# Performance work log

Hardware: AMD Instinct MI355X
Metric: run time of the kernel (lower is better)

The kernel has to match this reference:

```python
import jax, jax.numpy as jnp
import numpy as np

HIDDEN = 1024
HEADS = 16
HEAD_DIM = HIDDEN // HEADS
EPS = 1e-5


def setup_inputs() -> dict:
    key = jax.random.key(0)
    ks = jax.random.split(key, 12)
    B, S, H = 2, 2048, HIDDEN
    s = 1.0 / np.sqrt(H)
    x = jax.random.normal(ks[0], (B, S, H), dtype=jnp.float32)
    Wq = jax.random.normal(ks[1], (H, H), dtype=jnp.float32) * s
    bq = jnp.zeros((H,), dtype=jnp.float32)
    Wk = jax.random.normal(ks[2], (H, H), dtype=jnp.float32) * s
    bk = jnp.zeros((H,), dtype=jnp.float32)
    Wv = jax.random.normal(ks[3], (H, H), dtype=jnp.float32) * s
    bv = jnp.zeros((H,), dtype=jnp.float32)
    Wg = jax.random.normal(ks[4], (2 * H, H), dtype=jnp.float32) * (1.0 / np.sqrt(2 * H))
    bg = jnp.zeros((H,), dtype=jnp.float32)
    gamma = jnp.ones((H,), dtype=jnp.float32)
    beta = jnp.zeros((H,), dtype=jnp.float32)
    return {"x": x, "Wq": Wq, "bq": bq, "Wk": Wk, "bk": bk, "Wv": Wv, "bv": bv,
            "Wg": Wg, "bg": bg, "gamma": gamma, "beta": beta}


def reference(x, Wq, bq, Wk, bk, Wv, bv, Wg, bg, gamma, beta):
    B, S, H = x.shape
    def heads(t):  # [B,S,H] -> [B,nH,S,hd]
        return t.reshape(B, S, HEADS, HEAD_DIM).transpose(0, 2, 1, 3)
    Q = heads(x @ Wq + bq)
    K = heads(x @ Wk + bk)
    V = heads(x @ Wv + bv)
    scores = jnp.einsum('bhqd,bhkd->bhqk', Q, K) / jnp.sqrt(jnp.float32(HEAD_DIM))
    flow = scores - scores.transpose(0, 1, 3, 2)  # antisymmetric
    w = jax.nn.softmax(flow, axis=-1)
    flowed = jnp.einsum('bhqk,bhkd->bhqd', w, V)
    flowed = flowed.transpose(0, 2, 1, 3).reshape(B, S, H)
    gate = jax.nn.sigmoid(jnp.concatenate([x, flowed], axis=-1) @ Wg + bg)
    y = x + gate * flowed
    mu = jnp.mean(y, axis=-1, keepdims=True)
    var = jnp.mean(jnp.square(y - mu), axis=-1, keepdims=True)
    return (y - mu) * jax.lax.rsqrt(var + EPS) * gamma + beta
```

## Files before the change

kernel.cpp:

```cpp
#include <hip/hip_runtime.h>
#include <hip/hip_bf16.h>

#define S_LEN 2048
#define NHEAD 16
#define HDIM 64
#define HID 1024

typedef __attribute__((ext_vector_type(8))) short bf16x8;
typedef __attribute__((ext_vector_type(4))) float f32x4;
typedef __attribute__((ext_vector_type(4))) unsigned int u32x4;
typedef __attribute__((ext_vector_type(2))) unsigned int u32x2;

__device__ __forceinline__ unsigned short f2bf(float x) {
    unsigned int u = __builtin_bit_cast(unsigned int, x);
    u = (u + 0x7fffu + ((u >> 16) & 1u)) >> 16;
    return (unsigned short)u;
}
__device__ __forceinline__ float bf2f(unsigned short s) {
    unsigned int u = ((unsigned int)s) << 16;
    return __builtin_bit_cast(float, u);
}
__device__ __forceinline__ unsigned cvtpk_bf16(float lo, float hi) {
    unsigned r;
    asm("v_cvt_pk_bf16_f32 %0, %1, %2" : "=v"(r) : "v"(lo), "v"(hi));
    return r;
}
__device__ __forceinline__ void gload16(const short* g, short* l) {
    __builtin_amdgcn_global_load_lds(
        (const __attribute__((address_space(1))) unsigned int*)g,
        (__attribute__((address_space(3))) unsigned int*)l, 16, 0, 0);
}
__device__ __forceinline__ bf16x8 negbf8(bf16x8 v) {
    u32x4 u = __builtin_bit_cast(u32x4, v);
    #pragma unroll
    for (int e = 0; e < 4; e++) u[e] ^= 0x80008000u;
    return __builtin_bit_cast(bf16x8, u);
}

#define QSCALE 0.1803368801111168f

__global__ void cvt_kernel(const float* __restrict__ src, short* __restrict__ dst, int n4) {
    int i = blockIdx.x * blockDim.x + threadIdx.x;
    if (i < n4) {
        float4 v = reinterpret_cast<const float4*>(src)[i];
        short4 o;
        o.x = (short)f2bf(v.x); o.y = (short)f2bf(v.y);
        o.z = (short)f2bf(v.z); o.w = (short)f2bf(v.w);
        reinterpret_cast<short4*>(dst)[i] = o;
    }
}

__global__ void transpose_all(const float* __restrict__ Wq, const float* __restrict__ Wk,
                              const float* __restrict__ Wv, const float* __restrict__ Wg,
                              short* __restrict__ WT, short* __restrict__ WgT) {
    __shared__ float tile[32][33];
    int z = blockIdx.z;
    const float* src; short* dst; int R;
    if (z == 0)      { src = Wq; dst = WT;               R = 1024; }
    else if (z == 1) { src = Wk; dst = WT + 1024 * 1024; R = 1024; }
    else if (z == 2) { src = Wv; dst = WT + 2 * 1024 * 1024; R = 1024; }
    else             { src = Wg; dst = WgT;              R = 2048; }
    int by = blockIdx.y * 32;
    if (by >= R) return;
    int bx = blockIdx.x * 32;
    const int C = 1024;
    int tx = threadIdx.x, ty = threadIdx.y;
    #pragma unroll
    for (int i = ty; i < 32; i += 8)
        tile[i][tx] = src[(size_t)(by + i) * C + bx + tx];
    __syncthreads();
    #pragma unroll
    for (int i = ty; i < 32; i += 8)
        dst[(size_t)(bx + i) * R + by + tx] = (short)f2bf(tile[tx][i]);
}

__global__ __launch_bounds__(256, 2)
void gemm_qkv(const short* __restrict__ xb, const short* __restrict__ WT,
              const float* __restrict__ bq, const float* __restrict__ bk,
              const float* __restrict__ bv,
              short* __restrict__ Qb, short* __restrict__ Kb, short* __restrict__ VT) {
    __shared__ short Al[2][128 * 32];
    __shared__ short Bl[2][128 * 32];
    int mb = blockIdx.x, nb = blockIdx.y;
    int tid = threadIdx.x;
    int wave = tid >> 6, lane = tid & 63;
    int wm = wave >> 1, wn = wave & 1;
    int lr = lane & 15, lg = lane >> 4;

    int r = tid >> 2;
    int c = tid & 3;
    int sc = (c ^ (r & 3)) * 8;
    int dst0 = tid * 8;
    int dst1 = (tid + 256) * 8;
    const short* a0 = xb + (size_t)(mb * 128 + r) * 1024 + sc;
    const short* a1 = a0 + (size_t)64 * 1024;
    const short* b0 = WT + (size_t)(nb * 128 + r) * 1024 + sc;
    const short* b1 = b0 + (size_t)64 * 1024;
    int fsw = (lg ^ (lr & 3)) * 8;

    f32x4 acc[4][4] = {};

    for (int ks = 0; ks < 16; ++ks) {
        int kg = ks * 64;
        __syncthreads();
        gload16(a0 + kg,      &Al[0][dst0]);
        gload16(a1 + kg,      &Al[0][dst1]);
        gload16(a0 + kg + 32, &Al[1][dst0]);
        gload16(a1 + kg + 32, &Al[1][dst1]);
        gload16(b0 + kg,      &Bl[0][dst0]);
        gload16(b1 + kg,      &Bl[0][dst1]);
        gload16(b0 + kg + 32, &Bl[1][dst0]);
        gload16(b1 + kg + 32, &Bl[1][dst1]);
        __syncthreads();
        #pragma unroll
        for (int s = 0; s < 2; s++) {
            bf16x8 af[4], bfr[4];
            #pragma unroll
            for (int t = 0; t < 4; t++)
                af[t] = *(bf16x8*)&Al[s][(wm * 64 + t * 16 + lr) * 32 + fsw];
            #pragma unroll
            for (int t = 0; t < 4; t++)
                bfr[t] = *(bf16x8*)&Bl[s][(wn * 64 + t * 16 + lr) * 32 + fsw];
            #pragma unroll
            for (int i = 0; i < 4; i++)
                #pragma unroll
                for (int jn = 0; jn < 4; jn++)
                    acc[i][jn] = __builtin_amdgcn_mfma_f32_16x16x32_bf16(af[i], bfr[jn], acc[i][jn], 0, 0, 0);
        }
    }

    int which = (nb * 128) >> 10;
    #pragma unroll
    for (int jn = 0; jn < 4; jn++) {
        int n = nb * 128 + wn * 64 + jn * 16 + lr;
        int n1 = n & 1023;
        if (which < 2) {
            const float* bias = (which == 0) ? bq : bk;
            short* out = (which == 0) ? Qb : Kb;
            float scale = (which == 0) ? QSCALE : 1.0f;
            float bv_ = bias[n1];
            #pragma unroll
            for (int i = 0; i < 4; i++) {
                #pragma unroll
                for (int j = 0; j < 4; j++) {
                    int mm = mb * 128 + wm * 64 + i * 16 + lg * 4 + j;
                    out[(size_t)mm * 1024 + n1] = (short)f2bf(acc[i][jn][j] * scale + bv_ * scale);
                }
            }
        } else {
            int h = n1 >> 6, dv = n1 & 63;
            float bv_ = bv[n1];
            #pragma unroll
            for (int i = 0; i < 4; i++) {
                int mm0 = mb * 128 + wm * 64 + i * 16 + lg * 4;
                int bb = mm0 >> 11, ss = mm0 & 2047;
                short4 vvv;
                vvv.x = (short)f2bf(acc[i][jn][0] + bv_);
                vvv.y = (short)f2bf(acc[i][jn][1] + bv_);
                vvv.z = (short)f2bf(acc[i][jn][2] + bv_);
                vvv.w = (short)f2bf(acc[i][jn][3] + bv_);
                *(short4*)&VT[((size_t)((bb * 16 + h) * 64 + dv)) * S_LEN + ss] = vvv;
            }
        }
    }
}

__global__ __launch_bounds__(256, 4)
void attn_kernel(const short* __restrict__ Qb, const short* __restrict__ Kb,
                 const short* __restrict__ VT, short* __restrict__ Fb) {
    __shared__ short Kt[64 * 64];
    __shared__ short Qt[64 * 64];
    __shared__ short Vt[64 * 64];
    __shared__ short Pl[4][16 * 64];

    int bid = (blockIdx.x & 7) * 128 + (blockIdx.x >> 3);
    int qb = bid & 31;
    int bh = bid >> 5;
    int b = bh >> 4, h = bh & 15;
    int tid = threadIdx.x;
    int wave = tid >> 6, lane = tid & 63;
    int lr = lane & 15, lg = lane >> 4;

    size_t rowbase = ((size_t)(b * S_LEN + qb * 64 + wave * 16 + lr)) * HID + h * HDIM;
    bf16x8 Qf[2], Kf[2];
    #pragma unroll
    for (int cc = 0; cc < 2; cc++) {
        Qf[cc] = *(const bf16x8*)(Qb + rowbase + cc * 32 + lg * 8);
        Kf[cc] = negbf8(*(const bf16x8*)(Kb + rowbase + cc * 32 + lg * 8));
    }

    int r0 = tid >> 3;
    int c = tid & 7;
    int swz = (c ^ (r0 & 7)) * 8;
    int dst0 = r0 * 64 + swz;
    int dst1 = (r0 + 32) * 64 + swz;
    const short* kp = Kb + (size_t)(b * S_LEN + r0) * HID + h * HDIM + c * 8;
    const short* qp = Qb + (size_t)(b * S_LEN + r0) * HID + h * HDIM + c * 8;
    const short* vp = VT + (size_t)bh * HDIM * S_LEN + (size_t)r0 * S_LEN + c * 8;

    bf16x8 kv0 = *(const bf16x8*)kp;
    bf16x8 kv1 = *(const bf16x8*)(kp + 32 * HID);
    bf16x8 qv0 = *(const bf16x8*)qp;
    bf16x8 qv1 = *(const bf16x8*)(qp + 32 * HID);
    bf16x8 vv0 = *(const bf16x8*)vp;
    bf16x8 vv1 = *(const bf16x8*)(vp + 32 * S_LEN);
    kp += 64 * HID; qp += 64 * HID; vp += 64;

    f32x4 O[4] = {};
    float m = -1e30f, l = 0.f;

    for (int kt = 0; kt < 32; ++kt) {
        __syncthreads();
        *(bf16x8*)&Kt[dst0] = kv0;
        *(bf16x8*)&Kt[dst1] = kv1;
        *(bf16x8*)&Qt[dst0] = qv0;
        *(bf16x8*)&Qt[dst1] = qv1;
        *(bf16x8*)&Vt[dst0] = vv0;
        *(bf16x8*)&Vt[dst1] = vv1;
        __syncthreads();

        if (kt < 31) {
            kv0 = *(const bf16x8*)kp;
            kv1 = *(const bf16x8*)(kp + 32 * HID);
            qv0 = *(const bf16x8*)qp;
            qv1 = *(const bf16x8*)(qp + 32 * HID);
            vv0 = *(const bf16x8*)vp;
            vv1 = *(const bf16x8*)(vp + 32 * S_LEN);
            kp += 64 * HID; qp += 64 * HID; vp += 64;
        }

        f32x4 S[4] = {};
        __builtin_amdgcn_s_setprio(1);
        #pragma unroll
        for (int t = 0; t < 4; t++) {
            #pragma unroll
            for (int c2 = 0; c2 < 2; c2++) {
                int fo = (t * 16 + lr) * 64 + (((4 * c2 + lg) ^ (lr & 7)) * 8);
                bf16x8 kf = *(bf16x8*)&Kt[fo];
                bf16x8 qf = *(bf16x8*)&Qt[fo];
                S[t] = __builtin_amdgcn_mfma_f32_16x16x32_bf16(kf, Qf[c2], S[t], 0, 0, 0);
                S[t] = __builtin_amdgcn_mfma_f32_16x16x32_bf16(qf, Kf[c2], S[t], 0, 0, 0);
            }
        }
        __builtin_amdgcn_s_setprio(0);

        float pm = -1e30f;
        #pragma unroll
        for (int t = 0; t < 4; t++)
            #pragma unroll
            for (int j = 0; j < 4; j++) pm = fmaxf(pm, S[t][j]);
        pm = fmaxf(pm, __shfl_xor(pm, 16));
        pm = fmaxf(pm, __shfl_xor(pm, 32));

        if (__any(pm > m + 8.f)) {
            float mn = fmaxf(m, pm);
            float alpha = exp2f(m - mn);
            m = mn;
            l *= alpha;
            float a[4];
            #pragma unroll
            for (int j = 0; j < 4; j++) a[j] = __shfl(alpha, lg * 4 + j);
            #pragma unroll
            for (int dvt = 0; dvt < 4; dvt++)
                #pragma unroll
                for (int j = 0; j < 4; j++) O[dvt][j] *= a[j];
        }

        unsigned Pd[4][2];
        float rs = 0.f;
        #pragma unroll
        for (int t = 0; t < 4; t++) {
            float p0 = exp2f(S[t][0] - m);
            float p1 = exp2f(S[t][1] - m);
            float p2 = exp2f(S[t][2] - m);
            float p3 = exp2f(S[t][3] - m);
            rs += (p0 + p1) + (p2 + p3);
            Pd[t][0] = cvtpk_bf16(p0, p1);
            Pd[t][1] = cvtpk_bf16(p2, p3);
        }
        rs += __shfl_xor(rs, 16);
        rs += __shfl_xor(rs, 32);
        l += rs;
        #pragma unroll
        for (int t = 0; t < 4; t++) {
            u32x2 pw;
            pw[0] = Pd[t][0];
            pw[1] = Pd[t][1];
            int po = lr * 64 + (((2 * t + (lg >> 1)) ^ (lr & 7)) * 8) + (lg & 1) * 4;
            *(u32x2*)&Pl[wave][po] = pw;
        }

        __builtin_amdgcn_s_setprio(1);
        #pragma unroll
        for (int c2 = 0; c2 < 2; c2++) {
            bf16x8 pf = *(bf16x8*)&Pl[wave][lr * 64 + (((4 * c2 + lg) ^ (lr & 7)) * 8)];
            #pragma unroll
            for (int dvt = 0; dvt < 4; dvt++) {
                bf16x8 vf = *(bf16x8*)&Vt[(dvt * 16 + lr) * 64 + (((4 * c2 + lg) ^ (lr & 7)) * 8)];
                O[dvt] = __builtin_amdgcn_mfma_f32_16x16x32_bf16(pf, vf, O[dvt], 0, 0, 0);
            }
        }
        __builtin_amdgcn_s_setprio(0);
    }

    float linv = 1.f / l;
    float li[4];
    #pragma unroll
    for (int j = 0; j < 4; j++) li[j] = __shfl(linv, lg * 4 + j);
    #pragma unroll
    for (int dvt = 0; dvt < 4; dvt++) {
        #pragma unroll
        for (int j = 0; j < 4; j++) {
            int q = qb * 64 + wave * 16 + lg * 4 + j;
            int dv = dvt * 16 + lr;
            Fb[((size_t)(b * S_LEN + q)) * HID + h * HDIM + dv] =
                (short)f2bf(O[dvt][j] * li[j]);
        }
    }
}

__global__ __launch_bounds__(256, 4)
void gemm_gate(const short* __restrict__ xb, const short* __restrict__ fb,
               const short* __restrict__ WgT, const float* __restrict__ bg,
               const float* __restrict__ x, float* __restrict__ y) {
    __shared__ short Al[2][64 * 32];
    __shared__ short Bl[2][64 * 32];
    int mb = blockIdx.x, nb = blockIdx.y;
    int tid = threadIdx.x;
    int wave = tid >> 6, lane = tid & 63;
    int wm = wave >> 1, wn = wave & 1;
    int lr = lane & 15, lg = lane >> 4;

    int r = tid >> 2;
    int c = tid & 3;
    int sc = (c ^ (r & 3)) * 8;
    int dst0 = tid * 8;
    size_t arow = (size_t)(mb * 64 + r) * 1024 + sc;
    const short* b0 = WgT + (size_t)(nb * 64 + r) * 2048 + sc;
    int fsw = (lg ^ (lr & 3)) * 8;

    f32x4 acc[2][2] = {};

    for (int ks = 0; ks < 32; ++ks) {
        int kg = ks * 64;
        const short* A = (kg < 1024) ? (xb + kg) : (fb + (kg - 1024));
        __syncthreads();
        gload16(A + arow, &Al[0][dst0]);
        gload16(A + arow + 32, &Al[1][dst0]);
        gload16(b0 + kg, &Bl[0][dst0]);
        gload16(b0 + kg + 32, &Bl[1][dst0]);
        __syncthreads();
        bf16x8 af[2][2], bfr[2][2];
        #pragma unroll
        for (int t = 0; t < 2; t++)
            #pragma unroll
            for (int s = 0; s < 2; s++) {
                af[t][s]  = *(bf16x8*)&Al[s][(wm * 32 + t * 16 + lr) * 32 + fsw];
                bfr[t][s] = *(bf16x8*)&Bl[s][(wn * 32 + t * 16 + lr) * 32 + fsw];
            }
        #pragma unroll
        for (int i = 0; i < 2; i++)
            #pragma unroll
            for (int jn = 0; jn < 2; jn++)
                #pragma unroll
                for (int s = 0; s < 2; s++)
                    acc[i][jn] = __builtin_amdgcn_mfma_f32_16x16x32_bf16(af[i][s], bfr[jn][s], acc[i][jn], 0, 0, 0);
    }

    #pragma unroll
    for (int jn = 0; jn < 2; jn++) {
        int n = nb * 64 + wn * 32 + jn * 16 + lr;
        float bgv = bg[n];
        #pragma unroll
        for (int i = 0; i < 2; i++) {
            #pragma unroll
            for (int j = 0; j < 4; j++) {
                int mm = mb * 64 + wm * 32 + i * 16 + lg * 4 + j;
                size_t idx = (size_t)mm * 1024 + n;
                float z = acc[i][jn][j] + bgv;
                float gate = 1.f / (1.f + __expf(-z));
                float fv = bf2f((unsigned short)fb[idx]);
                y[idx] = x[idx] + gate * fv;
            }
        }
    }
}

__global__ __launch_bounds__(256)
void ln_kernel(float* __restrict__ y, const float* __restrict__ gamma,
               const float* __restrict__ beta) {
    int row = blockIdx.x;
    int tid = threadIdx.x;
    float4 v4 = *(const float4*)&y[(size_t)row * 1024 + tid * 4];
    float v[4] = {v4.x, v4.y, v4.z, v4.w};
    float s = v[0] + v[1] + v[2] + v[3];
    float s2 = v[0]*v[0] + v[1]*v[1] + v[2]*v[2] + v[3]*v[3];
    #pragma unroll
    for (int off = 1; off < 64; off <<= 1) {
        s += __shfl_xor(s, off);
        s2 += __shfl_xor(s2, off);
    }
    __shared__ float red[8];
    int wave = tid >> 6, lane = tid & 63;
    if (lane == 0) { red[wave] = s; red[4 + wave] = s2; }
    __syncthreads();
    s = red[0] + red[1] + red[2] + red[3];
    s2 = red[4] + red[5] + red[6] + red[7];
    float mu = s * (1.f / 1024.f);
    float var = s2 * (1.f / 1024.f) - mu * mu;
    float rsq = rsqrtf(var + 1e-5f);
    float4 o4;
    float* o = (float*)&o4;
    #pragma unroll
    for (int e = 0; e < 4; e++) {
        int n = tid * 4 + e;
        o[e] = (v[e] - mu) * rsq * gamma[n] + beta[n];
    }
    *(float4*)&y[(size_t)row * 1024 + tid * 4] = o4;
}

extern "C" void kernel_launch(void* const* d_in, const int* in_sizes, int n_in,
                              void* d_out, int out_size, void* d_ws, size_t ws_size,
                              hipStream_t stream) {
    const float* x     = (const float*)d_in[0];
    const float* Wq    = (const float*)d_in[1];
    const float* bq    = (const float*)d_in[2];
    const float* Wk    = (const float*)d_in[3];
    const float* bk    = (const float*)d_in[4];
    const float* Wv    = (const float*)d_in[5];
    const float* bv    = (const float*)d_in[6];
    const float* Wg    = (const float*)d_in[7];
    const float* bg    = (const float*)d_in[8];
    const float* gamma = (const float*)d_in[9];
    const float* beta  = (const float*)d_in[10];
    float* out = (float*)d_out;

    char* w = (char*)d_ws;
    const size_t MB = 1024 * 1024;
    short* xb  = (short*)(w + 0 * MB);
    short* Qb  = (short*)(w + 8 * MB);
    short* Kb  = (short*)(w + 16 * MB);
    short* WT  = (short*)(w + 32 * MB);
    short* WgT = (short*)(w + 38 * MB);
    short* fb  = (short*)(w + 42 * MB);
    short* VT  = (short*)(w + 50 * MB);

    cvt_kernel<<<4096, 256, 0, stream>>>(x, xb, 4096 * 1024 / 4);
    dim3 tb(32, 8);
    transpose_all<<<dim3(32, 64, 4), tb, 0, stream>>>(Wq, Wk, Wv, Wg, WT, WgT);
    gemm_qkv<<<dim3(32, 24), 256, 0, stream>>>(xb, WT, bq, bk, bv, Qb, Kb, VT);
    attn_kernel<<<1024, 256, 0, stream>>>(Qb, Kb, VT, fb);
    gemm_gate<<<dim3(64, 16), 256, 0, stream>>>(xb, fb, WgT, bg, x, out);
    ln_kernel<<<4096, 256, 0, stream>>>(out, gamma, beta);
}
```

Before: 171.3 us.

## Double-buffer K/Q shared tiles and restructure attention loop synchronization

Splits the K and Q shared-memory tiles into two buffers. The next tile's K/Q is written into the alternate buffer while the current one feeds the score MFMAs, and the global prefetch is moved to after the score computation. Barriers now sit between the P store and the PV product, and at the end of each iteration, instead of around the tile stores. The goal is to let the QK^T MFMAs start without waiting on a barrier after the stores. In exchange it uses more LDS, and it issues unconditional prefetches past the last tile, which read beyond the sequence and possibly beyond the buffer end.

```diff
diff --git a/kernel.cpp b/kernel.cpp
--- a/kernel.cpp
+++ b/kernel.cpp
@@ -168,8 +168,8 @@
 __global__ __launch_bounds__(256, 4)
 void attn_kernel(const short* __restrict__ Qb, const short* __restrict__ Kb,
                  const short* __restrict__ VT, short* __restrict__ Fb) {
-    __shared__ short Kt[64 * 64];
-    __shared__ short Qt[64 * 64];
+    __shared__ short Kt[2][64 * 64];
+    __shared__ short Qt[2][64 * 64];
     __shared__ short Vt[64 * 64];
     __shared__ short Pl[4][16 * 64];
 
@@ -204,30 +204,30 @@
     bf16x8 qv1 = *(const bf16x8*)(qp + 32 * HID);
     bf16x8 vv0 = *(const bf16x8*)vp;
     bf16x8 vv1 = *(const bf16x8*)(vp + 32 * S_LEN);
+    *(bf16x8*)&Kt[0][dst0] = kv0;
+    *(bf16x8*)&Kt[0][dst1] = kv1;
+    *(bf16x8*)&Qt[0][dst0] = qv0;
+    *(bf16x8*)&Qt[0][dst1] = qv1;
     kp += 64 * HID; qp += 64 * HID; vp += 64;
+    kv0 = *(const bf16x8*)kp;
+    kv1 = *(const bf16x8*)(kp + 32 * HID);
+    qv0 = *(const bf16x8*)qp;
+    qv1 = *(const bf16x8*)(qp + 32 * HID);
+    kp += 64 * HID; qp += 64 * HID;
 
     f32x4 O[4] = {};
     float m = -1e30f, l = 0.f;
+    int pb = 0;
+
+    __syncthreads();
 
     for (int kt = 0; kt < 32; ++kt) {
-        __syncthreads();
-        *(bf16x8*)&Kt[dst0] = kv0;
-        *(bf16x8*)&Kt[dst1] = kv1;
-        *(bf16x8*)&Qt[dst0] = qv0;
-        *(bf16x8*)&Qt[dst1] = qv1;
         *(bf16x8*)&Vt[dst0] = vv0;
         *(bf16x8*)&Vt[dst1] = vv1;
-        __syncthreads();
-
-        if (kt < 31) {
-            kv0 = *(const bf16x8*)kp;
-            kv1 = *(const bf16x8*)(kp + 32 * HID);
-            qv0 = *(const bf16x8*)qp;
-            qv1 = *(const bf16x8*)(qp + 32 * HID);
-            vv0 = *(const bf16x8*)vp;
-            vv1 = *(const bf16x8*)(vp + 32 * S_LEN);
-            kp += 64 * HID; qp += 64 * HID; vp += 64;
-        }
+        *(bf16x8*)&Kt[pb ^ 1][dst0] = kv0;
+        *(bf16x8*)&Kt[pb ^ 1][dst1] = kv1;
+        *(bf16x8*)&Qt[pb ^ 1][dst0] = qv0;
+        *(bf16x8*)&Qt[pb ^ 1][dst1] = qv1;
 
         f32x4 S[4] = {};
         __builtin_amdgcn_s_setprio(1);
@@ -236,13 +236,22 @@
             #pragma unroll
             for (int c2 = 0; c2 < 2; c2++) {
                 int fo = (t * 16 + lr) * 64 + (((4 * c2 + lg) ^ (lr & 7)) * 8);
-                bf16x8 kf = *(bf16x8*)&Kt[fo];
-                bf16x8 qf = *(bf16x8*)&Qt[fo];
+                bf16x8 kf = *(bf16x8*)&Kt[pb][fo];
+                bf16x8 qf = *(bf16x8*)&Qt[pb][fo];
                 S[t] = __builtin_amdgcn_mfma_f32_16x16x32_bf16(kf, Qf[c2], S[t], 0, 0, 0);
                 S[t] = __builtin_amdgcn_mfma_f32_16x16x32_bf16(qf, Kf[c2], S[t], 0, 0, 0);
             }
         }
         __builtin_amdgcn_s_setprio(0);
+
+        vv0 = *(const bf16x8*)vp;
+        vv1 = *(const bf16x8*)(vp + 32 * S_LEN);
+        vp += 64;
+        kv0 = *(const bf16x8*)kp;
+        kv1 = *(const bf16x8*)(kp + 32 * HID);
+        qv0 = *(const bf16x8*)qp;
+        qv1 = *(const bf16x8*)(qp + 32 * HID);
+        kp += 64 * HID; qp += 64 * HID;
 
         float pm = -1e30f;
         #pragma unroll
@@ -290,6 +299,8 @@
             *(u32x2*)&Pl[wave][po] = pw;
         }
 
+        __syncthreads();
+
         __builtin_amdgcn_s_setprio(1);
         #pragma unroll
         for (int c2 = 0; c2 < 2; c2++) {
@@ -301,6 +312,9 @@
             }
         }
         __builtin_amdgcn_s_setprio(0);
+
+        __syncthreads();
+        pb ^= 1;
     }
 
     float linv = 1.f / l;
```

Measured after the change: 185.2 us. 8.1% more time.
